# Performance work log

Hardware: AMD Instinct MI355X
Metric: run time of the kernel (lower is better)

## Reference

```python
import jax, jax.numpy as jnp
import numpy as np

N = 100000
E = 1600000
D_FEAT = 64
D_HID = 64
T = 20
DT = 0.5


def setup_inputs() -> dict:
    key = jax.random.key(0)
    ks = jax.random.split(key, 12)
    inp = {
        "S0": jax.random.uniform(ks[0], (N,), dtype=jnp.float32),
        "I0": jax.random.uniform(ks[1], (N,), dtype=jnp.float32),
        "R0": jnp.zeros((N,), dtype=jnp.float32),
        "time_grid": jnp.arange(T, dtype=jnp.float32),
        "node_feat": jax.random.normal(ks[2], (N, D_FEAT), dtype=jnp.float32),
        "edge_index": jax.random.randint(ks[3], (2, E), 0, N, dtype=jnp.int64),
        "edge_weight": jax.random.uniform(ks[4], (E,), dtype=jnp.float32),
        "W_msg": jax.random.normal(ks[5], (D_FEAT + 1, D_HID), dtype=jnp.float32) * 0.1,
        "W_self": jax.random.normal(ks[6], (D_FEAT + 1, D_HID), dtype=jnp.float32) * 0.1,
        "b_h": jnp.zeros((D_HID,), dtype=jnp.float32),
        "w_beta": jax.random.normal(ks[7], (D_HID,), dtype=jnp.float32) * 0.1,
        "b_beta": jnp.zeros((1,), dtype=jnp.float32),
        "w_gamma": jax.random.normal(ks[8], (D_HID,), dtype=jnp.float32) * 0.1,
        "b_gamma": jnp.zeros((1,), dtype=jnp.float32),
    }
    return inp


def reference(S0, I0, R0, time_grid, node_feat, edge_index, edge_weight,
              W_msg, W_self, b_h, w_beta, b_beta, w_gamma, b_gamma):
    n = S0.shape[0]
    src = edge_index[0]
    dst = edge_index[1]

    def step(carry, _):
        S, I, R = carry
        # gnn block: x_in = [node_feat, I]  -> [N, d_feat+1]
        x_in = jnp.concatenate([node_feat, I[:, None]], axis=-1)
        # project first, then gather: (x_in @ W_msg)[src] is math-equivalent to x_in[src] @ W_msg
        msg = (x_in @ W_msg)[src] * edge_weight[:, None]          # [E, d_hid]
        agg = jax.ops.segment_sum(msg, dst, num_segments=n)       # [N, d_hid]
        h = jax.nn.relu(agg + x_in @ W_self + b_h)
        # param net: per-node beta/gamma
        beta = jax.nn.sigmoid(h @ w_beta + b_beta[0])             # [N]
        gamma = jax.nn.sigmoid(h @ w_gamma + b_gamma[0])          # [N]
        # edge scatter-add force
        force = jax.ops.segment_sum(edge_weight * I[src], dst, num_segments=n)
        force = jnp.clip(force, 0.0, 1000.0)
        inf = beta * S * force
        rec = gamma * I
        S = jnp.clip(S + (-inf) * DT, 0.0, 1.0)
        I = jnp.clip(I + (inf - rec) * DT, 0.0, 1.0)
        R = jnp.clip(R + rec * DT, 0.0, 1.0)
        return (S, I, R), (I, beta, gamma)

    (_, _, _), (I_seq, betas, gammas) = jax.lax.scan(
        step, (S0, I0, R0), None, length=time_grid.shape[0])
    return I_seq, betas[-1], gammas[-1]
```

## Files before the change

### kernel.cpp

```cpp
#include <hip/hip_runtime.h>
#include <hip/hip_fp16.h>
#include <cstdint>
#include <cstddef>

#define DT_F 0.5f
#define KF_CHUNKS 768
#define ELL_C 64

__global__ void detect_i64(const long long* __restrict__ ei, int E, int n,
                           int* __restrict__ flag) {
    __shared__ int ok;
    if (threadIdx.x == 0) ok = 1;
    __syncthreads();
    int m = E < 2048 ? E : 2048;
    for (int i = threadIdx.x; i < m; i += blockDim.x) {
        long long v = ei[i];
        if (v < 0 || v >= (long long)n) ok = 0;
    }
    __syncthreads();
    if (threadIdx.x == 0) flag[0] = ok;
}

__device__ __forceinline__ int ld_idx(const void* ei, size_t pos, int w64) {
    return w64 ? (int)((const long long*)ei)[pos] : ((const int*)ei)[pos];
}

__global__ void k_pack(const void* __restrict__ ei, const float* __restrict__ ew,
                       const int* __restrict__ flag, int E,
                       int* __restrict__ dst32, uint32_t* __restrict__ sw32,
                       int colbits, float scale) {
    int e = blockIdx.x * blockDim.x + threadIdx.x;
    if (e >= E) return;
    int w64 = flag[0];
    dst32[e] = ld_idx(ei, (size_t)E + e, w64);
    uint32_t w15 = (uint32_t)(ew[e] * scale + 0.5f);
    sw32[e] = (w15 << colbits) | (uint32_t)ld_idx(ei, e, w64);
}

__global__ void k_fill_ell(const int* __restrict__ dst32,
                           const uint32_t* __restrict__ sw32,
                           int E, int n,
                           int* __restrict__ cnt,
                           uint32_t* __restrict__ ev) {
    int slice = blockIdx.x & 7;
    int chunk = blockIdx.x >> 3;
    int per = (E + KF_CHUNKS - 1) / KF_CHUNKS;
    int e0 = chunk * per;
    int e1 = e0 + per; if (e1 > E) e1 = E;
    int lo = (int)(((long long)n * slice) >> 3);
    int hi = (int)(((long long)n * (slice + 1)) >> 3);
    for (int e = e0 + (int)threadIdx.x; e < e1; e += blockDim.x) {
        int d = __builtin_nontemporal_load(&dst32[e]);
        if (d < lo || d >= hi) continue;
        int p = atomicAdd(&cnt[d], 1);
        if (p < ELL_C)
            ev[(size_t)d * ELL_C + p] = __builtin_nontemporal_load(&sw32[e]);
    }
}

__global__ void proj_tiled(const float* __restrict__ nf,
                           const float* __restrict__ Wm,
                           const float* __restrict__ Wsf,
                           const float* __restrict__ bh,
                           float* __restrict__ PM, float* __restrict__ HC,
                           int n) {
    __shared__ float sWmT[64 * 65];
    __shared__ float sWsT[64 * 65];
    __shared__ float sNf[64 * 68];
    for (int i = threadIdx.x; i < 64 * 64; i += 256) {
        int k = i >> 6, j = i & 63;
        sWmT[j * 65 + k] = Wm[i];
        sWsT[j * 65 + k] = Wsf[i];
    }
    int node0 = blockIdx.x * 64;
    for (int i = threadIdx.x; i < 64 * 64; i += 256) {
        int r = i >> 6, c = i & 63;
        if (node0 + r < n) sNf[r * 68 + c] = nf[(size_t)(node0 + r) * 64 + c];
    }
    __syncthreads();
    int w   = threadIdx.x >> 6;
    int j   = threadIdx.x & 63;
    float accm[16], accs[16];
#pragma unroll
    for (int ni = 0; ni < 16; ++ni) { accm[ni] = 0.f; accs[ni] = 0.f; }
    for (int kq = 0; kq < 16; ++kq) {
        int k = kq * 4;
        float wm0 = sWmT[j * 65 + k],     wm1 = sWmT[j * 65 + k + 1];
        float wm2 = sWmT[j * 65 + k + 2], wm3 = sWmT[j * 65 + k + 3];
        float ws0 = sWsT[j * 65 + k],     ws1 = sWsT[j * 65 + k + 1];
        float ws2 = sWsT[j * 65 + k + 2], ws3 = sWsT[j * 65 + k + 3];
#pragma unroll
        for (int ni = 0; ni < 16; ++ni) {
            float4 a = *(const float4*)&sNf[(w * 16 + ni) * 68 + k];
            accm[ni] = fmaf(a.w, wm3, fmaf(a.z, wm2, fmaf(a.y, wm1, fmaf(a.x, wm0, accm[ni]))));
            accs[ni] = fmaf(a.w, ws3, fmaf(a.z, ws2, fmaf(a.y, ws1, fmaf(a.x, ws0, accs[ni]))));
        }
    }
    float bhl = bh[j];
#pragma unroll
    for (int ni = 0; ni < 16; ++ni) {
        int node = node0 + w * 16 + ni;
        if (node < n) {
            PM[(size_t)node * 64 + j] = accm[ni];
            HC[(size_t)node * 64 + j] = accs[ni] + bhl;
        }
    }
}

__global__ void edge_wide_ell(const int* __restrict__ cnt,
                              const uint32_t* __restrict__ ev,
                              const float* __restrict__ PM,
                              const float* __restrict__ HCin,
                              __half* __restrict__ HCh, int n,
                              int colbits, float inv_scale) {
    int wave = (blockIdx.x * blockDim.x + threadIdx.x) >> 6;
    int lane = threadIdx.x & 63;
    if (wave >= n) return;
    uint32_t cmask = (1u << colbits) - 1;
    int deg = cnt[wave]; if (deg > ELL_C) deg = ELL_C;
    int d4 = (deg + 3) & ~3;
    const uint32_t* row = ev + (size_t)wave * ELL_C;
    float acc0 = 0.f, acc1 = 0.f, acc2 = 0.f, acc3 = 0.f;
    for (int e = 0; e < d4; e += 4) {
        uint4 q = *(const uint4*)&row[e];
        float v0 = PM[(size_t)(q.x & cmask) * 64 + lane];
        float v1 = PM[(size_t)(q.y & cmask) * 64 + lane];
        float v2 = PM[(size_t)(q.z & cmask) * 64 + lane];
        float v3 = PM[(size_t)(q.w & cmask) * 64 + lane];
        acc0 = fmaf((float)(q.x >> colbits) * inv_scale, v0, acc0);
        acc1 = fmaf((float)(q.y >> colbits) * inv_scale, v1, acc1);
        acc2 = fmaf((float)(q.z >> colbits) * inv_scale, v2, acc2);
        acc3 = fmaf((float)(q.w >> colbits) * inv_scale, v3, acc3);
    }
    size_t o = (size_t)wave * 64 + lane;
    HCh[o] = __float2half(HCin[o] + ((acc0 + acc1) + (acc2 + acc3)));
}

__global__ void step_fused4(const int* __restrict__ cnt,
                            const uint32_t* __restrict__ ev,
                            const __half2* __restrict__ HCh2,
                            const float4* __restrict__ wmL4,
                            const float4* __restrict__ wsL4,
                            const float4* __restrict__ wb4, const float* __restrict__ bb,
                            const float4* __restrict__ wg4, const float* __restrict__ bg,
                            const float* __restrict__ I_old,
                            float* __restrict__ S,
                            float* __restrict__ Iseq_t,
                            float* __restrict__ beta_out, float* __restrict__ gamma_out,
                            int n, int last, int colbits, float inv_scale) {
    int wid  = (blockIdx.x * blockDim.x + threadIdx.x) >> 6;
    int lane = threadIdx.x & 63;
    int l16  = lane & 15;
    int node = wid * 4 + (lane >> 4);
    if (node >= n) return;
    uint32_t cmask = (1u << colbits) - 1;
    int deg = cnt[node]; if (deg > ELL_C) deg = ELL_C;
    const uint32_t* row = ev + (size_t)node * ELL_C;
    float f = 0.f;
    for (int e = l16; e < deg; e += 16) {
        uint32_t p = row[e];
        f = fmaf((float)(p >> colbits) * inv_scale, I_old[p & cmask], f);
    }
    f += __shfl_xor(f, 1); f += __shfl_xor(f, 2);
    f += __shfl_xor(f, 4); f += __shfl_xor(f, 8);
    float Iv = I_old[node];
    __half2 hA = HCh2[(size_t)node * 32 + l16 * 2];
    __half2 hB = HCh2[(size_t)node * 32 + l16 * 2 + 1];
    float2 fA = __half22float2(hA);
    float2 fB = __half22float2(hB);
    float4 wm = wmL4[l16], wsv = wsL4[l16];
    float4 h;
    h.x = fmaxf(fmaf(f, wm.x, fmaf(Iv, wsv.x, fA.x)), 0.f);
    h.y = fmaxf(fmaf(f, wm.y, fmaf(Iv, wsv.y, fA.y)), 0.f);
    h.z = fmaxf(fmaf(f, wm.z, fmaf(Iv, wsv.z, fB.x)), 0.f);
    h.w = fmaxf(fmaf(f, wm.w, fmaf(Iv, wsv.w, fB.y)), 0.f);
    float4 wbv = wb4[l16], wgv = wg4[l16];
    float pb = fmaf(h.x, wbv.x, fmaf(h.y, wbv.y, fmaf(h.z, wbv.z, h.w * wbv.w)));
    float pg = fmaf(h.x, wgv.x, fmaf(h.y, wgv.y, fmaf(h.z, wgv.z, h.w * wgv.w)));
    pb += __shfl_xor(pb, 1); pg += __shfl_xor(pg, 1);
    pb += __shfl_xor(pb, 2); pg += __shfl_xor(pg, 2);
    pb += __shfl_xor(pb, 4); pg += __shfl_xor(pg, 4);
    pb += __shfl_xor(pb, 8); pg += __shfl_xor(pg, 8);
    if (l16 == 0) {
        float beta  = 1.f / (1.f + expf(-(pb + bb[0])));
        float gamma = 1.f / (1.f + expf(-(pg + bg[0])));
        float fc = fminf(fmaxf(f, 0.f), 1000.f);
        float Sv = S[node];
        float inf_ = beta * Sv * fc;
        float rec  = gamma * Iv;
        float Sn = fminf(fmaxf(Sv - inf_ * DT_F, 0.f), 1.f);
        float In = fminf(fmaxf(Iv + (inf_ - rec) * DT_F, 0.f), 1.f);
        S[node] = Sn;
        Iseq_t[node] = In;
        if (last) { beta_out[node] = beta; gamma_out[node] = gamma; }
    }
}

extern "C" void kernel_launch(void* const* d_in, const int* in_sizes, int n_in,
                              void* d_out, int out_size, void* d_ws, size_t ws_size,
                              hipStream_t stream) {
    const float* S0  = (const float*)d_in[0];
    const float* I0  = (const float*)d_in[1];
    const float* nf  = (const float*)d_in[4];
    const void*  ei  = d_in[5];
    const float* ew  = (const float*)d_in[6];
    const float* Wm  = (const float*)d_in[7];
    const float* Wsf = (const float*)d_in[8];
    const float* bh  = (const float*)d_in[9];
    const float* wb  = (const float*)d_in[10];
    const float* bb  = (const float*)d_in[11];
    const float* wg  = (const float*)d_in[12];
    const float* bg  = (const float*)d_in[13];

    const int n = in_sizes[0];
    const int T = in_sizes[3];
    const int E = in_sizes[6];

    int colbits = 1;
    while ((1 << colbits) < n) ++colbits;
    float scale = (float)((1u << (32 - colbits)) - 1);
    float inv_scale = 1.0f / scale;

    char* ws = (char*)d_ws;
    size_t off = 0;
    auto alloc = [&](size_t bytes) {
        size_t p = off;
        off = (off + bytes + 255) & ~(size_t)255;
        return p;
    };
    float*  HC     = (float*)(ws + alloc((size_t)n * 64 * 4));
    float*  PM     = (float*)(ws + alloc((size_t)n * 64 * 4));
    __half* HCh    = (__half*)(ws + alloc((size_t)n * 64 * 2));
    float*  S      = (float*)(ws + alloc((size_t)n * 4));
    int*    cnt    = (int*)(ws + alloc((size_t)n * 4));
    uint32_t* ev   = (uint32_t*)(ws + alloc((size_t)n * ELL_C * 4));
    int*    dst32  = (int*)(ws + alloc((size_t)E * 4));
    uint32_t* sw32 = (uint32_t*)(ws + alloc((size_t)E * 4));
    int*    flag   = (int*)(ws + alloc(256));
    if (off > ws_size) return;

    float* out       = (float*)d_out;
    float* beta_out  = out + (size_t)T * n;
    float* gamma_out = out + (size_t)T * n + n;

    hipMemcpyAsync(S, S0, (size_t)n * 4, hipMemcpyDeviceToDevice, stream);
    hipMemsetAsync(cnt, 0, (size_t)n * 4, stream);
    hipMemsetAsync(ev, 0, (size_t)n * ELL_C * 4, stream);

    detect_i64<<<1, 256, 0, stream>>>((const long long*)ei, E, n, flag);
    k_pack<<<(E + 255) / 256, 256, 0, stream>>>(ei, ew, flag, E, dst32, sw32,
                                                colbits, scale);
    k_fill_ell<<<KF_CHUNKS * 8, 256, 0, stream>>>(dst32, sw32, E, n, cnt, ev);

    proj_tiled<<<(n + 63) / 64, 256, 0, stream>>>(nf, Wm, Wsf, bh, PM, HC, n);
    edge_wide_ell<<<(n * 64 + 255) / 256, 256, 0, stream>>>(
        cnt, ev, PM, HC, HCh, n, colbits, inv_scale);

    const __half2* HCh2 = (const __half2*)HCh;
    const float4* wmL4 = (const float4*)(Wm  + 64 * 64);
    const float4* wsL4 = (const float4*)(Wsf + 64 * 64);
    const float4* wb4  = (const float4*)wb;
    const float4* wg4  = (const float4*)wg;
    int swaves = (n + 3) / 4;
    int sblocks = (swaves * 64 + 255) / 256;
    for (int t = 0; t < T; ++t) {
        const float* Iold = (t == 0) ? I0 : out + (size_t)(t - 1) * n;
        step_fused4<<<sblocks, 256, 0, stream>>>(
            cnt, ev, HCh2, wmL4, wsL4, wb4, bb, wg4, bg,
            Iold, S, out + (size_t)t * n, beta_out, gamma_out,
            n, t == T - 1 ? 1 : 0, colbits, inv_scale);
    }
}
```

Measured before the change: 520.5 us.

## Bin edges by destination slice in shared memory before ELL scatter

Replaces the pack pass plus the 8-way sliced fill pass with a single binning kernel. It reads the edges once and groups them into 8 destination slices in LDS staging buffers. A second kernel then does the atomic ELL insertion per slice for locality. The full ELL memset is dropped, and edge_wide_ell now handles the degree tail exactly instead of relying on zeroed padding. The risk is that other readers (step_fused4) may still read padded entries, which are no longer zeroed.

```diff
diff --git a/kernel.cpp b/kernel.cpp
--- a/kernel.cpp
+++ b/kernel.cpp
@@ -4,8 +4,10 @@
 #include <cstddef>
 
 #define DT_F 0.5f
-#define KF_CHUNKS 768
 #define ELL_C 64
+#define NBIN 768
+#define BCAP 512
+#define NSC 96
 
 __global__ void detect_i64(const long long* __restrict__ ei, int E, int n,
                            int* __restrict__ flag) {
@@ -25,36 +27,70 @@
     return w64 ? (int)((const long long*)ei)[pos] : ((const int*)ei)[pos];
 }
 
-__global__ void k_pack(const void* __restrict__ ei, const float* __restrict__ ew,
-                       const int* __restrict__ flag, int E,
-                       int* __restrict__ dst32, uint32_t* __restrict__ sw32,
-                       int colbits, float scale) {
-    int e = blockIdx.x * blockDim.x + threadIdx.x;
-    if (e >= E) return;
+__global__ void k_bin(const void* __restrict__ ei, const float* __restrict__ ew,
+                      const int* __restrict__ flag, int E, int n,
+                      int colbits, float scale,
+                      int2* __restrict__ staging, int scap,
+                      int* __restrict__ gcur,
+                      int* __restrict__ cnt, uint32_t* __restrict__ ev) {
+    __shared__ int2 bins[8][BCAP];
+    __shared__ int bcnt[8];
+    __shared__ int gbase[8];
+    int tid = threadIdx.x;
+    if (tid < 8) bcnt[tid] = 0;
+    __syncthreads();
+    int per = (E + NBIN - 1) / NBIN;
+    int e0 = blockIdx.x * per;
+    int e1 = e0 + per; if (e1 > E) e1 = E;
     int w64 = flag[0];
-    dst32[e] = ld_idx(ei, (size_t)E + e, w64);
-    uint32_t w15 = (uint32_t)(ew[e] * scale + 0.5f);
-    sw32[e] = (w15 << colbits) | (uint32_t)ld_idx(ei, e, w64);
-}
-
-__global__ void k_fill_ell(const int* __restrict__ dst32,
-                           const uint32_t* __restrict__ sw32,
-                           int E, int n,
-                           int* __restrict__ cnt,
-                           uint32_t* __restrict__ ev) {
-    int slice = blockIdx.x & 7;
-    int chunk = blockIdx.x >> 3;
-    int per = (E + KF_CHUNKS - 1) / KF_CHUNKS;
-    int e0 = chunk * per;
-    int e1 = e0 + per; if (e1 > E) e1 = E;
-    int lo = (int)(((long long)n * slice) >> 3);
-    int hi = (int)(((long long)n * (slice + 1)) >> 3);
-    for (int e = e0 + (int)threadIdx.x; e < e1; e += blockDim.x) {
-        int d = __builtin_nontemporal_load(&dst32[e]);
-        if (d < lo || d >= hi) continue;
-        int p = atomicAdd(&cnt[d], 1);
-        if (p < ELL_C)
-            ev[(size_t)d * ELL_C + p] = __builtin_nontemporal_load(&sw32[e]);
+    for (int e = e0 + tid; e < e1; e += blockDim.x) {
+        int d = ld_idx(ei, (size_t)E + e, w64);
+        uint32_t w15 = (uint32_t)(ew[e] * scale + 0.5f);
+        uint32_t sw = (w15 << colbits) | (uint32_t)ld_idx(ei, e, w64);
+        int s = (int)(((long long)d * 8) / n);
+        int p = atomicAdd(&bcnt[s], 1);
+        if (p < BCAP) {
+            bins[s][p] = make_int2(d, (int)sw);
+        } else {
+            int q = atomicAdd(&cnt[d], 1);
+            if (q < ELL_C) ev[(size_t)d * ELL_C + q] = sw;
+        }
+    }
+    __syncthreads();
+    if (tid < 8) {
+        int c = bcnt[tid]; if (c > BCAP) c = BCAP;
+        bcnt[tid] = c;
+        gbase[tid] = atomicAdd(&gcur[tid], c);
+    }
+    __syncthreads();
+    for (int s = 0; s < 8; ++s) {
+        int c = bcnt[s], gb = gbase[s];
+        for (int i = tid; i < c; i += blockDim.x) {
+            int pos = gb + i;
+            if (pos < scap) {
+                staging[(size_t)s * scap + pos] = bins[s][i];
+            } else {
+                int2 t = bins[s][i];
+                int q = atomicAdd(&cnt[t.x], 1);
+                if (q < ELL_C) ev[(size_t)t.x * ELL_C + q] = (uint32_t)t.y;
+            }
+        }
+    }
+}
+
+__global__ void k_scatter(const int2* __restrict__ staging, int scap,
+                          const int* __restrict__ gcur,
+                          int* __restrict__ cnt, uint32_t* __restrict__ ev) {
+    int s   = blockIdx.x & 7;
+    int blk = blockIdx.x >> 3;
+    int tot = gcur[s]; if (tot > scap) tot = scap;
+    int per = (tot + NSC - 1) / NSC;
+    int i0 = blk * per;
+    int i1 = i0 + per; if (i1 > tot) i1 = tot;
+    for (int i = i0 + (int)threadIdx.x; i < i1; i += blockDim.x) {
+        int2 t = staging[(size_t)s * scap + i];
+        int p = atomicAdd(&cnt[t.x], 1);
+        if (p < ELL_C) ev[(size_t)t.x * ELL_C + p] = (uint32_t)t.y;
     }
 }
 
@@ -118,7 +154,7 @@
     if (wave >= n) return;
     uint32_t cmask = (1u << colbits) - 1;
     int deg = cnt[wave]; if (deg > ELL_C) deg = ELL_C;
-    int d4 = (deg + 3) & ~3;
+    int d4 = deg & ~3;
     const uint32_t* row = ev + (size_t)wave * ELL_C;
     float acc0 = 0.f, acc1 = 0.f, acc2 = 0.f, acc3 = 0.f;
     for (int e = 0; e < d4; e += 4) {
@@ -131,6 +167,11 @@
         acc1 = fmaf((float)(q.y >> colbits) * inv_scale, v1, acc1);
         acc2 = fmaf((float)(q.z >> colbits) * inv_scale, v2, acc2);
         acc3 = fmaf((float)(q.w >> colbits) * inv_scale, v3, acc3);
+    }
+    for (int e = d4; e < deg; ++e) {
+        uint32_t q = row[e];
+        acc0 = fmaf((float)(q >> colbits) * inv_scale,
+                    PM[(size_t)(q & cmask) * 64 + lane], acc0);
     }
     size_t o = (size_t)wave * 64 + lane;
     HCh[o] = __float2half(HCin[o] + ((acc0 + acc1) + (acc2 + acc3)));
@@ -220,6 +261,7 @@
     while ((1 << colbits) < n) ++colbits;
     float scale = (float)((1u << (32 - colbits)) - 1);
     float inv_scale = 1.0f / scale;
+    const int scap = E / 4 + 65536;
 
     char* ws = (char*)d_ws;
     size_t off = 0;
@@ -228,15 +270,15 @@
         off = (off + bytes + 255) & ~(size_t)255;
         return p;
     };
-    float*  HC     = (float*)(ws + alloc((size_t)n * 64 * 4));
-    float*  PM     = (float*)(ws + alloc((size_t)n * 64 * 4));
-    __half* HCh    = (__half*)(ws + alloc((size_t)n * 64 * 2));
-    float*  S      = (float*)(ws + alloc((size_t)n * 4));
-    int*    cnt    = (int*)(ws + alloc((size_t)n * 4));
-    uint32_t* ev   = (uint32_t*)(ws + alloc((size_t)n * ELL_C * 4));
-    int*    dst32  = (int*)(ws + alloc((size_t)E * 4));
-    uint32_t* sw32 = (uint32_t*)(ws + alloc((size_t)E * 4));
-    int*    flag   = (int*)(ws + alloc(256));
+    float*  HC      = (float*)(ws + alloc((size_t)n * 64 * 4));
+    float*  PM      = (float*)(ws + alloc((size_t)n * 64 * 4));
+    __half* HCh     = (__half*)(ws + alloc((size_t)n * 64 * 2));
+    float*  S       = (float*)(ws + alloc((size_t)n * 4));
+    int*    cnt     = (int*)(ws + alloc((size_t)n * 4));
+    uint32_t* ev    = (uint32_t*)(ws + alloc((size_t)n * ELL_C * 4));
+    int2*   staging = (int2*)(ws + alloc((size_t)8 * scap * 8));
+    int*    gcur    = (int*)(ws + alloc(256));
+    int*    flag    = (int*)(ws + alloc(256));
     if (off > ws_size) return;
 
     float* out       = (float*)d_out;
@@ -245,12 +287,12 @@
 
     hipMemcpyAsync(S, S0, (size_t)n * 4, hipMemcpyDeviceToDevice, stream);
     hipMemsetAsync(cnt, 0, (size_t)n * 4, stream);
-    hipMemsetAsync(ev, 0, (size_t)n * ELL_C * 4, stream);
+    hipMemsetAsync(gcur, 0, 256, stream);
 
     detect_i64<<<1, 256, 0, stream>>>((const long long*)ei, E, n, flag);
-    k_pack<<<(E + 255) / 256, 256, 0, stream>>>(ei, ew, flag, E, dst32, sw32,
-                                                colbits, scale);
-    k_fill_ell<<<KF_CHUNKS * 8, 256, 0, stream>>>(dst32, sw32, E, n, cnt, ev);
+    k_bin<<<NBIN, 256, 0, stream>>>(ei, ew, flag, E, n, colbits, scale,
+                                    staging, scap, gcur, cnt, ev);
+    k_scatter<<<NSC * 8, 256, 0, stream>>>(staging, scap, gcur, cnt, ev);
 
     proj_tiled<<<(n + 63) / 64, 256, 0, stream>>>(nf, Wm, Wsf, bh, PM, HC, n);
     edge_wide_ell<<<(n * 64 + 255) / 256, 256, 0, stream>>>(
```

New measurement: 513.3 us. Within noise of the previous version (-1.4%).
